# Optimization experiments

Measured on AMD Instinct MI355X. Metric: run time of the kernel, lower is better.

The kernel has to match this reference:

```python
import jax, jax.numpy as jnp
import numpy as np

N_NODES = 200   # sensors
SEQ = 128       # sequence_length == d_model of per-node transformers
BATCH = 256     # transformer treats batch as the attention sequence (2D input)
HEADS = 4
LAYERS = 2
NF = 1          # num_features (forced to 1 by fc dims)
F_OUT = 64      # num_out_features
G_OUT = 64      # gnn_output_dim
N_EDGES = 1600
D = SEQ
EPS = 1e-5


def setup_inputs() -> dict:
    key = jax.random.key(0)
    ks = jax.random.split(key, 20)
    s = 0.05
    nrm = lambda k, shp: jax.random.normal(k, shp, jnp.float32) * s
    return {
        "x": jax.random.normal(ks[0], (BATCH, N_NODES, SEQ), jnp.float32),
        "edge_index": jax.random.randint(ks[1], (2, N_EDGES), 0, N_NODES),
        # per-node, per-layer transformer params (stacked for vmap)
        "Wqkv": nrm(ks[2], (N_NODES, LAYERS, 3 * D, D)),
        "bqkv": nrm(ks[3], (N_NODES, LAYERS, 3 * D)),
        "Wo": nrm(ks[4], (N_NODES, LAYERS, D, D)),
        "bo": nrm(ks[5], (N_NODES, LAYERS, D)),
        "g1": jnp.ones((N_NODES, LAYERS, D), jnp.float32),
        "be1": jnp.zeros((N_NODES, LAYERS, D), jnp.float32),
        "fW1": nrm(ks[6], (N_NODES, LAYERS, D, D)),  # dim_feedforward = SEQ = D
        "fb1": nrm(ks[7], (N_NODES, LAYERS, D)),
        "fW2": nrm(ks[8], (N_NODES, LAYERS, D, D)),
        "fb2": nrm(ks[9], (N_NODES, LAYERS, D)),
        "g2": jnp.ones((N_NODES, LAYERS, D), jnp.float32),
        "be2": jnp.zeros((N_NODES, LAYERS, D), jnp.float32),
        # shared fc: Linear(SEQ*NF, F_OUT)
        "fc_W": nrm(ks[10], (F_OUT, SEQ * NF)),
        "fc_b": nrm(ks[11], (F_OUT,)),
        # GATConv(F_OUT, G_OUT), heads=1
        "gat_W": nrm(ks[12], (G_OUT, F_OUT)),
        "att_src": nrm(ks[13], (G_OUT,)),
        "att_dst": nrm(ks[14], (G_OUT,)),
        "gat_b": nrm(ks[15], (G_OUT,)),
        # predictor Linear(G_OUT, 2)
        "pred_W": nrm(ks[16], (2, G_OUT)),
        "pred_b": nrm(ks[17], (2,)),
    }


def _ln(v, g, b):
    m = v.mean(-1, keepdims=True)
    var = ((v - m) ** 2).mean(-1, keepdims=True)
    return (v - m) / jnp.sqrt(var + EPS) * g + b


def _encoder_one_node(xn, Wqkv, bqkv, Wo, bo, g1, be1, fW1, fb1, fW2, fb2, g2, be2):
    # xn: [S, D] with S = BATCH (torch treats the 2D input as unbatched seq)
    dh = D // HEADS
    scale = jnp.asarray(1.0 / np.sqrt(dh), xn.dtype)
    for l in range(LAYERS):  # post-norm TransformerEncoderLayer, relu, no dropout (eval)
        qkv = xn @ Wqkv[l].T + bqkv[l]                    # [S, 3D]
        q, k, v = jnp.split(qkv, 3, axis=-1)
        q = q.reshape(-1, HEADS, dh)
        k = k.reshape(-1, HEADS, dh)
        v = v.reshape(-1, HEADS, dh)
        s = jnp.einsum('qhd,khd->hqk', q, k) * scale      # [H, S, S]
        a = jax.nn.softmax(s, axis=-1)
        o = jnp.einsum('hqk,khd->qhd', a, v).reshape(-1, D)
        o = o @ Wo[l].T + bo[l]
        xn = _ln(xn + o, g1[l], be1[l])
        f = jax.nn.relu(xn @ fW1[l].T + fb1[l]) @ fW2[l].T + fb2[l]
        xn = _ln(xn + f, g2[l], be2[l])
    return xn


def _forward(edge_index, x, Wqkv, bqkv, Wo, bo, g1, be1, fW1, fb1, fW2, fb2, g2, be2,
             fc_W, fc_b, gat_W, att_src, att_dst, gat_b, pred_W, pred_b):
    B, N, _ = x.shape
    xt = jnp.transpose(x, (1, 0, 2))                      # [N, B, D]
    t_out = jax.vmap(_encoder_one_node)(xt, Wqkv, bqkv, Wo, bo, g1, be1,
                                        fW1, fb1, fW2, fb2, g2, be2)  # [N, B, D]
    feat = t_out @ fc_W.T + fc_b                          # [N, B, F_OUT]
    # replicate torch.cat(dim=0) over nodes followed by .view(B, N, F)
    feat = feat.reshape(N * B, F_OUT).reshape(B, N, F_OUT)

    # GATConv with add_self_loops, heads=1, negative_slope=0.2
    loops = jnp.arange(N, dtype=edge_index.dtype)
    src = jnp.concatenate([edge_index[0], loops])
    dst = jnp.concatenate([edge_index[1], loops])

    def gat(h_in):  # h_in: [N, F_OUT]
        h = h_in @ gat_W.T                                # [N, G_OUT]
        a_s = h @ att_src                                 # [N]
        a_d = h @ att_dst
        e = jax.nn.leaky_relu(a_s[src] + a_d[dst], 0.2)   # [E+N]
        emax = jax.ops.segment_max(e, dst, num_segments=N)
        emax = jnp.where(jnp.isfinite(emax), emax, 0.0)
        w = jnp.exp(e - emax[dst])
        denom = jax.ops.segment_sum(w, dst, num_segments=N)
        alpha = w / (denom[dst] + 1e-16)
        return jax.ops.segment_sum(alpha[:, None] * h[src], dst, num_segments=N) + gat_b

    g = jax.vmap(gat)(feat)                               # [B, N, G_OUT]
    return g @ pred_W.T + pred_b                          # [B, N, 2]


def reference(x, edge_index, Wqkv, bqkv, Wo, bo, g1, be1, fW1, fb1, fW2, fb2, g2, be2,
              fc_W, fc_b, gat_W, att_src, att_dst, gat_b, pred_W, pred_b):
    return _forward(edge_index, x, Wqkv, bqkv, Wo, bo, g1, be1, fW1, fb1, fW2, fb2,
                    g2, be2, fc_W, fc_b, gat_W, att_src, att_dst, gat_b, pred_W, pred_b)
```

## Files before the change

### kernel.cpp

```cpp
#include <hip/hip_runtime.h>
#include <hip/hip_bf16.h>

#define NN 200
#define BB 256
#define DD 128
#define DH 32
#define NE 1600
#define LL 2

typedef short short8 __attribute__((ext_vector_type(8)));
typedef short short4a __attribute__((ext_vector_type(4)));
typedef float floatx4 __attribute__((ext_vector_type(4)));
using bf16 = __hip_bfloat16;

__device__ __forceinline__ short bfs(float x) {
  bf16 h = __float2bfloat16(x);
  return *(short*)&h;
}
__device__ __forceinline__ float b2f(short s) {
  union { unsigned u; float f; } cv;
  cv.u = ((unsigned)(unsigned short)s) << 16;
  return cv.f;
}

__device__ __forceinline__ void swz_node(int bid, int per_node, int& node, int& rem) {
  int xcd = bid & 7;
  int slot = bid >> 3;
  int q = slot / per_node;
  node = xcd * (NN >> 3) + q;
  rem = slot - q * per_node;
}

__device__ __forceinline__ void stage_w(const float* __restrict__ wbase,
                                        short* WS, int tid) {
#pragma unroll
  for (int i = 0; i < 8; i++) {
    int idx = i * 256 + tid;
    float4 v = *(const float4*)(wbase + idx * 4);
    int rw = idx >> 5, k = (idx & 31) << 2;
    short4a p = {bfs(v.x), bfs(v.y), bfs(v.z), bfs(v.w)};
    *(short4a*)&WS[rw * 136 + k] = p;
  }
}

__device__ __forceinline__ void gemm_q(const short8* af, const short* WS, int r,
                                       int quad, floatx4* acc) {
#pragma unroll
  for (int k0 = 0; k0 < 4; k0++) {
#pragma unroll
    for (int s = 0; s < 4; s++) {
      short8 bq = *(const short8*)&WS[(s * 16 + r) * 136 + quad * 8 + k0 * 32];
      acc[s] = __builtin_amdgcn_mfma_f32_16x16x32_bf16(af[k0], bq, acc[s], 0, 0, 0);
    }
  }
}

__global__ __launch_bounds__(256) void k_transpose(const float* __restrict__ x,
                                                   bf16* __restrict__ X) {
  int tid = blockIdx.x * 256 + threadIdx.x;
  if (tid >= NN * BB * DD) return;
  int d = tid & (DD - 1);
  int rest = tid >> 7;
  int b = rest & (BB - 1);
  int node = rest >> 8;
  X[tid] = (bf16)x[((size_t)b * NN + node) * DD + d];
}

template <int MTPW>
__global__ __launch_bounds__(256) void k_gemm64(const bf16* __restrict__ A,
                                                const float* __restrict__ W,
                                                const float* __restrict__ bias,
                                                bf16* __restrict__ out, int nout,
                                                int astride, size_t woff, int wns,
                                                size_t boff, int bns, int relu,
                                                int nc_count) {
  __shared__ short WS[64 * 136];
  const int RSPLIT = 4 / MTPW;
  int per_node = nc_count * RSPLIT;
  int node, rem;
  swz_node(blockIdx.x, per_node, node, rem);
  int nc = rem / RSPLIT;
  int rh = rem - nc * RSPLIT;
  int tid = threadIdx.x;
  int w = tid >> 6, lane = tid & 63, r = lane & 15, quad = lane >> 4;
  int base_row = rh * 128 + w * (MTPW * 16);

  short8 areg[MTPW][4];
#pragma unroll
  for (int mt = 0; mt < MTPW; mt++) {
    const bf16* arow =
        A + ((size_t)node * BB + base_row + mt * 16 + r) * (size_t)astride + quad * 8;
#pragma unroll
    for (int k = 0; k < 4; k++) areg[mt][k] = *(const short8*)(arow + k * 32);
  }

  stage_w(W + woff + (size_t)node * (size_t)wns + (size_t)nc * 64 * DD, WS, tid);
  __syncthreads();

  floatx4 acc[MTPW][4];
  floatx4 z = {0.f, 0.f, 0.f, 0.f};
#pragma unroll
  for (int mt = 0; mt < MTPW; mt++)
#pragma unroll
    for (int s = 0; s < 4; s++) acc[mt][s] = z;

#pragma unroll
  for (int k0 = 0; k0 < 4; k0++) {
    short8 bq[4];
#pragma unroll
    for (int s = 0; s < 4; s++)
      bq[s] = *(const short8*)&WS[(s * 16 + r) * 136 + quad * 8 + k0 * 32];
#pragma unroll
    for (int mt = 0; mt < MTPW; mt++)
#pragma unroll
      for (int s = 0; s < 4; s++)
        acc[mt][s] = __builtin_amdgcn_mfma_f32_16x16x32_bf16(areg[mt][k0], bq[s],
                                                             acc[mt][s], 0, 0, 0);
  }

  const float* bp = bias + boff + (size_t)node * (size_t)bns + nc * 64;
  float bv[4];
#pragma unroll
  for (int s = 0; s < 4; s++) bv[s] = bp[s * 16 + r];

  __syncthreads();
  short* mybw = &WS[w * 1088];
  const size_t obase = (size_t)node * BB + base_row;
#pragma unroll
  for (int mt = 0; mt < MTPW; mt++) {
#pragma unroll
    for (int s = 0; s < 4; s++) {
#pragma unroll
      for (int i = 0; i < 4; i++) {
        float v = acc[mt][s][i] + bv[s];
        if (relu) v = v > 0.f ? v : 0.f;
        mybw[(quad * 4 + i) * 68 + s * 16 + r] = bfs(v);
      }
    }
#pragma unroll
    for (int j = 0; j < 2; j++) {
      int chunk = j * 64 + lane;
      int rowr = chunk >> 3, c8 = chunk & 7;
      short8 o = *(const short8*)&mybw[rowr * 68 + c8 * 8];
      *(short8*)((short*)out + (obase + mt * 16 + rowr) * (size_t)nout + nc * 64 + c8 * 8) = o;
    }
  }
}

__global__ __launch_bounds__(256) void k_ffn(const bf16* __restrict__ QKV,
                                             const float* __restrict__ Wo,
                                             const float* __restrict__ bo,
                                             bf16* __restrict__ X,
                                             const float* __restrict__ g1,
                                             const float* __restrict__ be1,
                                             const float* __restrict__ fW1,
                                             const float* __restrict__ fb1,
                                             const float* __restrict__ fW2,
                                             const float* __restrict__ fb2,
                                             const float* __restrict__ g2,
                                             const float* __restrict__ be2,
                                             size_t wso, int wns, size_t bso, int bns,
                                             int gstride,
                                             const float* __restrict__ W4,
                                             const float* __restrict__ C4,
                                             float* __restrict__ AS,
                                             float* __restrict__ ADv,
                                             float* __restrict__ HW0,
                                             float* __restrict__ HW1,
                                             int dofinal) {
  __shared__ short WS[64 * 136];
  __shared__ short HB[64 * 136];
  __shared__ short FB[64 * 136];
  int node, bt;
  swz_node(blockIdx.x, 4, node, bt);
  int tid = threadIdx.x;
  int w = tid >> 6, lane = tid & 63, r = lane & 15, quad = lane >> 4;
  int rrow = lane >> 2, cg = lane & 3;
  int row0 = bt * 64 + w * 16;

  const short* qrow = (const short*)QKV + ((size_t)node * BB + row0 + r) * 384 + quad * 8;
  short8 af[4];
#pragma unroll
  for (int k0 = 0; k0 < 4; k0++) af[k0] = *(const short8*)(qrow + k0 * 32);
  size_t xoff = ((size_t)node * BB + row0 + rrow) * DD + cg * 32;
  short8 xres[4];
#pragma unroll
  for (int c = 0; c < 4; c++) xres[c] = *(const short8*)((const short*)X + xoff + c * 8);

  floatx4 z = {0.f, 0.f, 0.f, 0.f};
  floatx4 acc[8];
  float vv[32];
  float bv[8];

  const float* WoN = Wo + wso + (size_t)node * (size_t)wns;
  stage_w(WoN, WS, tid);
  __syncthreads();
#pragma unroll
  for (int s = 0; s < 8; s++) acc[s] = z;
  gemm_q(af, WS, r, quad, &acc[0]);
  __syncthreads();
  stage_w(WoN + 64 * DD, WS, tid);
  __syncthreads();
  gemm_q(af, WS, r, quad, &acc[4]);

  const float* bpo = bo + bso + (size_t)node * (size_t)bns;
#pragma unroll
  for (int cch = 0; cch < 2; cch++)
#pragma unroll
    for (int s = 0; s < 4; s++) bv[cch * 4 + s] = bpo[cch * 64 + s * 16 + r];

  {
    float* BNC = (float*)&HB[w * 16 * 136];
#pragma unroll
    for (int s = 0; s < 4; s++)
#pragma unroll
      for (int i = 0; i < 4; i++)
        BNC[(quad * 4 + i) * 68 + s * 16 + r] = acc[s][i] + bv[s];
    if (cg < 2) {
#pragma unroll
      for (int j = 0; j < 8; j++) {
        float4 t4 = *(const float4*)&BNC[rrow * 68 + (cg & 1) * 32 + j * 4];
        vv[j * 4 + 0] = t4.x; vv[j * 4 + 1] = t4.y;
        vv[j * 4 + 2] = t4.z; vv[j * 4 + 3] = t4.w;
      }
    }
#pragma unroll
    for (int s = 0; s < 4; s++)
#pragma unroll
      for (int i = 0; i < 4; i++)
        BNC[(quad * 4 + i) * 68 + s * 16 + r] = acc[4 + s][i] + bv[4 + s];
    if (cg >= 2) {
#pragma unroll
      for (int j = 0; j < 8; j++) {
        float4 t4 = *(const float4*)&BNC[rrow * 68 + (cg & 1) * 32 + j * 4];
        vv[j * 4 + 0] = t4.x; vv[j * 4 + 1] = t4.y;
        vv[j * 4 + 2] = t4.z; vv[j * 4 + 3] = t4.w;
      }
    }
  }

  float sum = 0.f;
#pragma unroll
  for (int c = 0; c < 4; c++)
#pragma unroll
    for (int j = 0; j < 8; j++) {
      vv[c * 8 + j] += b2f(xres[c][j]);
      sum += vv[c * 8 + j];
    }
  sum += __shfl_xor(sum, 1);
  sum += __shfl_xor(sum, 2);
  float mean = sum * (1.0f / 128.0f);
  float vs = 0.f;
#pragma unroll
  for (int j = 0; j < 32; j++) {
    float d = vv[j] - mean;
    vs += d * d;
  }
  vs += __shfl_xor(vs, 1);
  vs += __shfl_xor(vs, 2);
  float inv = rsqrtf(vs * (1.0f / 128.0f) + 1e-5f);
  {
    const float* gp = g1 + bso + (size_t)node * gstride + cg * 32;
    const float* bep = be1 + bso + (size_t)node * gstride + cg * 32;
#pragma unroll
    for (int c = 0; c < 8; c++) {
      float4 g4 = *(const float4*)(gp + c * 4);
      float4 b4 = *(const float4*)(bep + c * 4);
      vv[c * 4 + 0] = (vv[c * 4 + 0] - mean) * inv * g4.x + b4.x;
      vv[c * 4 + 1] = (vv[c * 4 + 1] - mean) * inv * g4.y + b4.y;
      vv[c * 4 + 2] = (vv[c * 4 + 2] - mean) * inv * g4.z + b4.z;
      vv[c * 4 + 3] = (vv[c * 4 + 3] - mean) * inv * g4.w + b4.w;
    }
  }
  {
    short* hrow = &HB[(w * 16 + rrow) * 136 + cg * 32];
#pragma unroll
    for (int c = 0; c < 4; c++) {
      short8 hs;
#pragma unroll
      for (int j = 0; j < 8; j++) hs[j] = bfs(vv[c * 8 + j]);
      *(short8*)(hrow + c * 8) = hs;
    }
  }

  short8 hf[4];
#pragma unroll
  for (int k0 = 0; k0 < 4; k0++)
    hf[k0] = *(const short8*)&HB[(w * 16 + r) * 136 + quad * 8 + k0 * 32];
  __syncthreads();
  const float* W1N = fW1 + wso + (size_t)node * (size_t)wns;
  stage_w(W1N, WS, tid);
  __syncthreads();
#pragma unroll
  for (int s = 0; s < 8; s++) acc[s] = z;
  gemm_q(hf, WS, r, quad, &acc[0]);
  __syncthreads();
  stage_w(W1N + 64 * DD, WS, tid);
  __syncthreads();
  gemm_q(hf, WS, r, quad, &acc[4]);
  {
    const float* bp1 = fb1 + bso + (size_t)node * (size_t)bns;
#pragma unroll
    for (int cch = 0; cch < 2; cch++)
#pragma unroll
      for (int s = 0; s < 4; s++) {
        float bb = bp1[cch * 64 + s * 16 + r];
#pragma unroll
        for (int i = 0; i < 4; i++) {
          float v2 = acc[cch * 4 + s][i] + bb;
          FB[(w * 16 + quad * 4 + i) * 136 + cch * 64 + s * 16 + r] =
              bfs(v2 > 0.f ? v2 : 0.f);
        }
      }
  }

  __syncthreads();
  short8 ff[4];
#pragma unroll
  for (int k0 = 0; k0 < 4; k0++)
    ff[k0] = *(const short8*)&FB[(w * 16 + r) * 136 + quad * 8 + k0 * 32];
  const float* W2N = fW2 + wso + (size_t)node * (size_t)wns;
  stage_w(W2N, WS, tid);
  __syncthreads();
#pragma unroll
  for (int s = 0; s < 8; s++) acc[s] = z;
  gemm_q(ff, WS, r, quad, &acc[0]);
  __syncthreads();
  stage_w(W2N + 64 * DD, WS, tid);
  __syncthreads();
  gemm_q(ff, WS, r, quad, &acc[4]);

  const float* bp2 = fb2 + bso + (size_t)node * (size_t)bns;
#pragma unroll
  for (int cch = 0; cch < 2; cch++)
#pragma unroll
    for (int s = 0; s < 4; s++) bv[cch * 4 + s] = bp2[cch * 64 + s * 16 + r];

  {
    float* BNC = (float*)&FB[w * 16 * 136];
#pragma unroll
    for (int s = 0; s < 4; s++)
#pragma unroll
      for (int i = 0; i < 4; i++)
        BNC[(quad * 4 + i) * 68 + s * 16 + r] = acc[s][i] + bv[s];
    if (cg < 2) {
#pragma unroll
      for (int j = 0; j < 8; j++) {
        float4 t4 = *(const float4*)&BNC[rrow * 68 + (cg & 1) * 32 + j * 4];
        vv[j * 4 + 0] = t4.x; vv[j * 4 + 1] = t4.y;
        vv[j * 4 + 2] = t4.z; vv[j * 4 + 3] = t4.w;
      }
    }
#pragma unroll
    for (int s = 0; s < 4; s++)
#pragma unroll
      for (int i = 0; i < 4; i++)
        BNC[(quad * 4 + i) * 68 + s * 16 + r] = acc[4 + s][i] + bv[4 + s];
    if (cg >= 2) {
#pragma unroll
      for (int j = 0; j < 8; j++) {
        float4 t4 = *(const float4*)&BNC[rrow * 68 + (cg & 1) * 32 + j * 4];
        vv[j * 4 + 0] = t4.x; vv[j * 4 + 1] = t4.y;
        vv[j * 4 + 2] = t4.z; vv[j * 4 + 3] = t4.w;
      }
    }
  }

  sum = 0.f;
#pragma unroll
  for (int c = 0; c < 4; c++) {
    short8 hs = *(const short8*)&HB[(w * 16 + rrow) * 136 + cg * 32 + c * 8];
#pragma unroll
    for (int j = 0; j < 8; j++) {
      vv[c * 8 + j] += b2f(hs[j]);
      sum += vv[c * 8 + j];
    }
  }
  sum += __shfl_xor(sum, 1);
  sum += __shfl_xor(sum, 2);
  mean = sum * (1.0f / 128.0f);
  vs = 0.f;
#pragma unroll
  for (int j = 0; j < 32; j++) {
    float d = vv[j] - mean;
    vs += d * d;
  }
  vs += __shfl_xor(vs, 1);
  vs += __shfl_xor(vs, 2);
  inv = rsqrtf(vs * (1.0f / 128.0f) + 1e-5f);
  {
    const float* gp = g2 + bso + (size_t)node * gstride + cg * 32;
    const float* bep = be2 + bso + (size_t)node * gstride + cg * 32;
#pragma unroll
    for (int c = 0; c < 8; c++) {
      float4 g4 = *(const float4*)(gp + c * 4);
      float4 b4 = *(const float4*)(bep + c * 4);
      vv[c * 4 + 0] = (vv[c * 4 + 0] - mean) * inv * g4.x + b4.x;
      vv[c * 4 + 1] = (vv[c * 4 + 1] - mean) * inv * g4.y + b4.y;
      vv[c * 4 + 2] = (vv[c * 4 + 2] - mean) * inv * g4.z + b4.z;
      vv[c * 4 + 3] = (vv[c * 4 + 3] - mean) * inv * g4.w + b4.w;
    }
  }

  if (!dofinal) {
#pragma unroll
    for (int c = 0; c < 4; c++) {
      short8 os;
#pragma unroll
      for (int j = 0; j < 8; j++) os[j] = bfs(vv[c * 8 + j]);
      *(short8*)((short*)X + xoff + c * 8) = os;
    }
  } else {
    float a0 = 0.f, a1 = 0.f, a2 = 0.f, a3 = 0.f;
#pragma unroll
    for (int c = 0; c < 8; c++) {
      float4 w0 = *(const float4*)(W4 + cg * 32 + c * 4);
      float4 w1 = *(const float4*)(W4 + 128 + cg * 32 + c * 4);
      float4 w2 = *(const float4*)(W4 + 256 + cg * 32 + c * 4);
      float4 w3 = *(const float4*)(W4 + 384 + cg * 32 + c * 4);
      a0 += vv[c * 4] * w0.x + vv[c * 4 + 1] * w0.y + vv[c * 4 + 2] * w0.z + vv[c * 4 + 3] * w0.w;
      a1 += vv[c * 4] * w1.x + vv[c * 4 + 1] * w1.y + vv[c * 4 + 2] * w1.z + vv[c * 4 + 3] * w1.w;
      a2 += vv[c * 4] * w2.x + vv[c * 4 + 1] * w2.y + vv[c * 4 + 2] * w2.z + vv[c * 4 + 3] * w2.w;
      a3 += vv[c * 4] * w3.x + vv[c * 4 + 1] * w3.y + vv[c * 4 + 2] * w3.z + vv[c * 4 + 3] * w3.w;
    }
    a0 += __shfl_xor(a0, 1); a0 += __shfl_xor(a0, 2);
    a1 += __shfl_xor(a1, 1); a1 += __shfl_xor(a1, 2);
    a2 += __shfl_xor(a2, 1); a2 += __shfl_xor(a2, 2);
    a3 += __shfl_xor(a3, 1); a3 += __shfl_xor(a3, 2);
    if (cg == 0) {
      int grow = node * BB + row0 + rrow;
      AS[grow] = a0 + C4[0];
      ADv[grow] = a1 + C4[1];
      HW0[grow] = a2 + C4[2];
      HW1[grow] = a3 + C4[3];
    }
  }
}

__global__ __launch_bounds__(256) void k_attn(bf16* __restrict__ QKV) {
  __shared__ short VT[32 * 264];
  __shared__ short Pw[4 * 2560];
  int node, h;
  swz_node(blockIdx.x, 4, node, h);
  int tid = threadIdx.x;
  int wave = tid >> 6, lane = tid & 63, quad = lane >> 4, l15 = lane & 15;
  short* sbase = (short*)(QKV + (size_t)node * BB * 384);

  int q0 = wave * 64;
  short8 qf[4];
#pragma unroll
  for (int qt = 0; qt < 4; qt++)
    qf[qt] = *(const short8*)(sbase + (size_t)(q0 + qt * 16 + l15) * 384 + h * 32 + quad * 8);

  for (int i = tid; i < 4096; i += 256) {
    int key = i >> 4, dp = (i & 15) << 1;
    int two = *(const int*)(sbase + (size_t)key * 384 + 256 + h * 32 + dp);
    VT[dp * 264 + key] = (short)(two & 0xffff);
    VT[(dp + 1) * 264 + key] = (short)(((unsigned)two) >> 16);
  }
  __syncthreads();

  floatx4 zz = {0.f, 0.f, 0.f, 0.f};
  floatx4 acc[2][4];
#pragma unroll
  for (int dt = 0; dt < 2; dt++)
#pragma unroll
    for (int qt = 0; qt < 4; qt++) acc[dt][qt] = zz;
  float lp[4] = {0.f, 0.f, 0.f, 0.f};
  const float scale = 0.17677669529663689f;
  short* mypw = &Pw[wave * 2560];

#define KADDR(kt) (const short8*)(sbase + (size_t)((kt) * 16 + l15) * 384 + 128 + h * 32 + quad * 8)
  short8 kfA = *KADDR(0);
  short8 kfB = *KADDR(1);

  for (int g = 0; g < 8; g++) {
    short8 vf0 = *(const short8*)(&VT[l15 * 264 + g * 32 + quad * 8]);
    short8 vf1 = *(const short8*)(&VT[(16 + l15) * 264 + g * 32 + quad * 8]);
    short8 nA = kfA, nB = kfB;
    if (g < 7) {
      nA = *KADDR(g * 2 + 2);
      nB = *KADDR(g * 2 + 3);
    }
#pragma unroll
    for (int sub = 0; sub < 2; sub++) {
      short8 kf = sub ? kfB : kfA;
#pragma unroll
      for (int qt = 0; qt < 4; qt++) {
        floatx4 st = __builtin_amdgcn_mfma_f32_16x16x32_bf16(kf, qf[qt], zz, 0, 0, 0);
        float e0 = __expf(st[0] * scale);
        float e1 = __expf(st[1] * scale);
        float e2 = __expf(st[2] * scale);
        float e3 = __expf(st[3] * scale);
        lp[qt] += (e0 + e1) + (e2 + e3);
        short4a p = {bfs(e0), bfs(e1), bfs(e2), bfs(e3)};
        *(short4a*)(mypw + qt * 640 + l15 * 40 + sub * 16 + quad * 4) = p;
      }
    }
#pragma unroll
    for (int qt = 0; qt < 4; qt++) {
      short8 pf = *(const short8*)(mypw + qt * 640 + l15 * 40 + quad * 8);
      acc[0][qt] = __builtin_amdgcn_mfma_f32_16x16x32_bf16(vf0, pf, acc[0][qt], 0, 0, 0);
      acc[1][qt] = __builtin_amdgcn_mfma_f32_16x16x32_bf16(vf1, pf, acc[1][qt], 0, 0, 0);
    }
    kfA = nA;
    kfB = nB;
  }
#undef KADDR

  float inv[4];
#pragma unroll
  for (int qt = 0; qt < 4; qt++) {
    float lq = lp[qt];
    lq += __shfl_xor(lq, 16);
    lq += __shfl_xor(lq, 32);
    inv[qt] = 1.0f / lq;
  }

#pragma unroll
  for (int qt = 0; qt < 4; qt++)
#pragma unroll
    for (int dt = 0; dt < 2; dt++)
#pragma unroll
      for (int i = 0; i < 4; i++)
        mypw[(qt * 16 + l15) * 40 + dt * 16 + quad * 4 + i] = bfs(acc[dt][qt][i] * inv[qt]);

#pragma unroll
  for (int r = 0; r < 4; r++) {
    int chunk = r * 64 + lane;
    int query = chunk >> 2, d8 = (chunk & 3) * 8;
    short8 o = *(const short8*)(mypw + query * 40 + d8);
    *(short8*)(sbase + (size_t)(q0 + query) * 384 + h * 32 + d8) = o;
  }
}

__global__ __launch_bounds__(256) void k_prep(const float* __restrict__ gatW,
                                              const float* __restrict__ attS,
                                              const float* __restrict__ attD,
                                              const float* __restrict__ predW,
                                              const float* __restrict__ fcW,
                                              const float* __restrict__ fcb,
                                              float* __restrict__ W4,
                                              float* __restrict__ C4) {
  __shared__ float U[4][64];
  int t = threadIdx.x;
  int tt = t >> 6, f = t & 63;
  float u = 0.f;
  if (tt == 0) {
    for (int g = 0; g < 64; g++) u += gatW[g * 64 + f] * attS[g];
  } else if (tt == 1) {
    for (int g = 0; g < 64; g++) u += gatW[g * 64 + f] * attD[g];
  } else if (tt == 2) {
    for (int g = 0; g < 64; g++) u += gatW[g * 64 + f] * predW[g];
  } else {
    for (int g = 0; g < 64; g++) u += gatW[g * 64 + f] * predW[64 + g];
  }
  U[tt][f] = u;
  __syncthreads();
  for (int idx = t; idx < 512; idx += 256) {
    int v = idx >> 7, d = idx & 127;
    float w = 0.f;
#pragma unroll
    for (int ff = 0; ff < 64; ff++) w += fcW[ff * 128 + d] * U[v][ff];
    W4[v * 128 + d] = w;
  }
  if (t < 4) {
    float c = 0.f;
#pragma unroll
    for (int ff = 0; ff < 64; ff++) c += fcb[ff] * U[t][ff];
    C4[t] = c;
  }
}

__global__ __launch_bounds__(256) void k_gat(const int* __restrict__ EI,
                                             const float* __restrict__ AS,
                                             const float* __restrict__ ADv,
                                             const float* __restrict__ HW0,
                                             const float* __restrict__ HW1,
                                             const float* __restrict__ gatB,
                                             const float* __restrict__ predW,
                                             const float* __restrict__ predB,
                                             float* __restrict__ OUT) {
  __shared__ float sAS[NN], sAD[NN], sH0[NN], sH1[NN];
  __shared__ float n0[NN], n1[NN], den[NN];
  __shared__ float cc[2];
  int b = blockIdx.x;
  int t = threadIdx.x;
  int base = b * NN;
  for (int i = t; i < NN; i += 256) {
    sAS[i] = AS[base + i];
    sAD[i] = ADv[base + i];
    sH0[i] = HW0[base + i];
    sH1[i] = HW1[base + i];
    n0[i] = 0.f;
    n1[i] = 0.f;
    den[i] = 0.f;
  }
  if (t < 64) {
    float p0 = gatB[t] * predW[t];
    float p1 = gatB[t] * predW[64 + t];
#pragma unroll
    for (int off = 32; off; off >>= 1) {
      p0 += __shfl_down(p0, off);
      p1 += __shfl_down(p1, off);
    }
    if (t == 0) {
      cc[0] = p0 + predB[0];
      cc[1] = p1 + predB[1];
    }
  }
  __syncthreads();

  for (int i = t; i < NE + NN; i += 256) {
    int s, d;
    if (i < NE) {
      s = EI[i];
      d = EI[NE + i];
    } else {
      s = d = i - NE;
    }
    float ev = sAS[s] + sAD[d];
    float lr = ev > 0.f ? ev : 0.2f * ev;
    float w = __expf(lr);
    atomicAdd(&n0[d], w * sH0[s]);
    atomicAdd(&n1[d], w * sH1[s]);
    atomicAdd(&den[d], w);
  }
  __syncthreads();

  for (int i = t; i < NN; i += 256) {
    float inv = 1.0f / (den[i] + 1e-16f);
    OUT[2 * (base + i)] = n0[i] * inv + cc[0];
    OUT[2 * (base + i) + 1] = n1[i] * inv + cc[1];
  }
}

extern "C" void kernel_launch(void* const* d_in, const int* in_sizes, int n_in,
                              void* d_out, int out_size, void* d_ws, size_t ws_size,
                              hipStream_t stream) {
  const float* x = (const float*)d_in[0];
  const int* ei = (const int*)d_in[1];
  const float* Wqkv = (const float*)d_in[2];
  const float* bqkv = (const float*)d_in[3];
  const float* Wo = (const float*)d_in[4];
  const float* bo = (const float*)d_in[5];
  const float* g1 = (const float*)d_in[6];
  const float* be1 = (const float*)d_in[7];
  const float* fW1 = (const float*)d_in[8];
  const float* fb1 = (const float*)d_in[9];
  const float* fW2 = (const float*)d_in[10];
  const float* fb2 = (const float*)d_in[11];
  const float* g2 = (const float*)d_in[12];
  const float* be2 = (const float*)d_in[13];
  const float* fcW = (const float*)d_in[14];
  const float* fcb = (const float*)d_in[15];
  const float* gatW = (const float*)d_in[16];
  const float* attS = (const float*)d_in[17];
  const float* attD = (const float*)d_in[18];
  const float* gatB = (const float*)d_in[19];
  const float* predW = (const float*)d_in[20];
  const float* predB = (const float*)d_in[21];

  const size_t NEED = 53477376;
  if (ws_size < NEED) return;

  char* ws = (char*)d_ws;
  bf16* X = (bf16*)(ws);
  bf16* QKV = (bf16*)(ws + 13107200);
  float* W4 = (float*)(ws + 52428800);
  float* C4 = (float*)(ws + 52430848);
  float* AS = (float*)(ws + 52431872);
  float* ADv = (float*)(ws + 52636672);
  float* HW0 = (float*)(ws + 52841472);
  float* HW1 = (float*)(ws + 53046272);

  k_prep<<<1, 256, 0, stream>>>(gatW, attS, attD, predW, fcW, fcb, W4, C4);
  k_transpose<<<25600, 256, 0, stream>>>(x, X);

  for (int l = 0; l < LL; l++) {
    size_t w3o = (size_t)l * 384 * DD, b3o = (size_t)l * 384;
    size_t wso = (size_t)l * DD * DD, bso = (size_t)l * DD;
    k_gemm64<4><<<6 * NN, 256, 0, stream>>>(X, Wqkv, bqkv, QKV, 384, DD,
                                            w3o, LL * 384 * DD, b3o, LL * 384, 0, 6);
    k_attn<<<NN * 4, 256, 0, stream>>>(QKV);
    k_ffn<<<4 * NN, 256, 0, stream>>>(QKV, Wo, bo, X, g1, be1, fW1, fb1, fW2, fb2,
                                      g2, be2, wso, LL * DD * DD, bso, LL * DD,
                                      LL * DD, W4, C4, AS, ADv, HW0, HW1,
                                      (l == LL - 1) ? 1 : 0);
  }

  k_gat<<<BB, 256, 0, stream>>>(ei, AS, ADv, HW0, HW1, gatB, predW, predB,
                                (float*)d_out);
}
```

Measured before the change: 438.1 us.

## Prefetch next weight tile into registers during GEMMs; vectorize V transpose loads

The post-attention kernel now issues the global loads for the next 64-row weight chunk (Wo, fW1, fW2) into registers before running the current MFMA GEMM. It stores them to shared memory after the next barrier, so global load latency overlaps compute and is no longer exposed at each stage. The attention kernel's V transpose now loads 8 bf16 values per thread with a vector load instead of pairs, in four unrolled iterations. The prefetch costs 32 extra VGPRs per thread, which may reduce occupancy.

```diff
diff --git a/kernel.cpp b/kernel.cpp
--- a/kernel.cpp
+++ b/kernel.cpp
@@ -31,16 +31,25 @@
   rem = slot - q * per_node;
 }
 
+__device__ __forceinline__ void ldw_regs(const float* __restrict__ wbase, int tid,
+                                         float4* vr) {
+#pragma unroll
+  for (int i = 0; i < 8; i++) vr[i] = *(const float4*)(wbase + (i * 256 + tid) * 4);
+}
+__device__ __forceinline__ void st_ws(const float4* vr, short* WS, int tid) {
+#pragma unroll
+  for (int i = 0; i < 8; i++) {
+    int idx = i * 256 + tid;
+    int rw = idx >> 5, k = (idx & 31) << 2;
+    short4a p = {bfs(vr[i].x), bfs(vr[i].y), bfs(vr[i].z), bfs(vr[i].w)};
+    *(short4a*)&WS[rw * 136 + k] = p;
+  }
+}
 __device__ __forceinline__ void stage_w(const float* __restrict__ wbase,
                                         short* WS, int tid) {
-#pragma unroll
-  for (int i = 0; i < 8; i++) {
-    int idx = i * 256 + tid;
-    float4 v = *(const float4*)(wbase + idx * 4);
-    int rw = idx >> 5, k = (idx & 31) << 2;
-    short4a p = {bfs(v.x), bfs(v.y), bfs(v.z), bfs(v.w)};
-    *(short4a*)&WS[rw * 136 + k] = p;
-  }
+  float4 vr[8];
+  ldw_regs(wbase, tid, vr);
+  st_ws(vr, WS, tid);
 }
 
 __device__ __forceinline__ void gemm_q(const short8* af, const short* WS, int r,
@@ -187,20 +196,27 @@
 #pragma unroll
   for (int c = 0; c < 4; c++) xres[c] = *(const short8*)((const short*)X + xoff + c * 8);
 
+  const float* WoN = Wo + wso + (size_t)node * (size_t)wns;
+  const float* W1N = fW1 + wso + (size_t)node * (size_t)wns;
+  const float* W2N = fW2 + wso + (size_t)node * (size_t)wns;
+
   floatx4 z = {0.f, 0.f, 0.f, 0.f};
   floatx4 acc[8];
   float vv[32];
   float bv[8];
-
-  const float* WoN = Wo + wso + (size_t)node * (size_t)wns;
-  stage_w(WoN, WS, tid);
-  __syncthreads();
+  float4 wreg[8];
+
+  ldw_regs(WoN, tid, wreg);
+  st_ws(wreg, WS, tid);
+  __syncthreads();
+  ldw_regs(WoN + 64 * DD, tid, wreg);
 #pragma unroll
   for (int s = 0; s < 8; s++) acc[s] = z;
   gemm_q(af, WS, r, quad, &acc[0]);
   __syncthreads();
-  stage_w(WoN + 64 * DD, WS, tid);
-  __syncthreads();
+  st_ws(wreg, WS, tid);
+  __syncthreads();
+  ldw_regs(W1N, tid, wreg);
   gemm_q(af, WS, r, quad, &acc[4]);
 
   const float* bpo = bo + bso + (size_t)node * (size_t)bns;
@@ -283,20 +299,21 @@
     }
   }
 
+  __syncthreads();
+  st_ws(wreg, WS, tid);
+  __syncthreads();
+  ldw_regs(W1N + 64 * DD, tid, wreg);
   short8 hf[4];
 #pragma unroll
   for (int k0 = 0; k0 < 4; k0++)
     hf[k0] = *(const short8*)&HB[(w * 16 + r) * 136 + quad * 8 + k0 * 32];
-  __syncthreads();
-  const float* W1N = fW1 + wso + (size_t)node * (size_t)wns;
-  stage_w(W1N, WS, tid);
-  __syncthreads();
 #pragma unroll
   for (int s = 0; s < 8; s++) acc[s] = z;
   gemm_q(hf, WS, r, quad, &acc[0]);
   __syncthreads();
-  stage_w(W1N + 64 * DD, WS, tid);
-  __syncthreads();
+  st_ws(wreg, WS, tid);
+  __syncthreads();
+  ldw_regs(W2N, tid, wreg);
   gemm_q(hf, WS, r, quad, &acc[4]);
   {
     const float* bp1 = fb1 + bso + (size_t)node * (size_t)bns;
@@ -315,18 +332,18 @@
   }
 
   __syncthreads();
+  st_ws(wreg, WS, tid);
+  __syncthreads();
+  ldw_regs(W2N + 64 * DD, tid, wreg);
   short8 ff[4];
 #pragma unroll
   for (int k0 = 0; k0 < 4; k0++)
     ff[k0] = *(const short8*)&FB[(w * 16 + r) * 136 + quad * 8 + k0 * 32];
-  const float* W2N = fW2 + wso + (size_t)node * (size_t)wns;
-  stage_w(W2N, WS, tid);
-  __syncthreads();
 #pragma unroll
   for (int s = 0; s < 8; s++) acc[s] = z;
   gemm_q(ff, WS, r, quad, &acc[0]);
   __syncthreads();
-  stage_w(W2N + 64 * DD, WS, tid);
+  st_ws(wreg, WS, tid);
   __syncthreads();
   gemm_q(ff, WS, r, quad, &acc[4]);
 
@@ -452,11 +469,13 @@
   for (int qt = 0; qt < 4; qt++)
     qf[qt] = *(const short8*)(sbase + (size_t)(q0 + qt * 16 + l15) * 384 + h * 32 + quad * 8);
 
-  for (int i = tid; i < 4096; i += 256) {
-    int key = i >> 4, dp = (i & 15) << 1;
-    int two = *(const int*)(sbase + (size_t)key * 384 + 256 + h * 32 + dp);
-    VT[dp * 264 + key] = (short)(two & 0xffff);
-    VT[(dp + 1) * 264 + key] = (short)(((unsigned)two) >> 16);
+#pragma unroll
+  for (int it = 0; it < 4; it++) {
+    int i = it * 256 + tid;
+    int key = i >> 2, dq = (i & 3) << 3;
+    short8 v8 = *(const short8*)(sbase + (size_t)key * 384 + 256 + h * 32 + dq);
+#pragma unroll
+    for (int j = 0; j < 8; j++) VT[(dq + j) * 264 + key] = v8[j];
   }
   __syncthreads();
 
```

After: 402.8 us. 1.09x faster.
